# Performance work log

Hardware: AMD Instinct MI355X
Metric: run time of the kernel (lower is better)

The kernel has to match this reference:

```python
import jax, jax.numpy as jnp
import numpy as np

B, S, N = 4, 512, 2048
E = 1024          # expanded_size
QL, H, D, VL = 32, 8, 2, 32   # query_len, num_heads, num_duplicates, values_len
EPS = 1e-5


def setup_inputs() -> dict:
    key = jax.random.key(0)
    ks = jax.random.split(key, 8)
    return {
        "embeddings": jax.random.normal(ks[0], (B, S, E), jnp.float32),
        "keys": jax.random.normal(ks[1], (B, N, QL * H), jnp.float32),
        "values": jax.random.normal(ks[2], (B, N, VL * H), jnp.float32),
        "output_connectivity_sub": jax.random.normal(ks[3], (H, S * D, N), jnp.float32),
        "Wq": jax.random.normal(ks[4], (QL * H * D, E), jnp.float32) / np.sqrt(E),
        "bq": jnp.zeros((QL * H * D,), jnp.float32),
        "Wo": jax.random.normal(ks[5], (E, VL * H * D), jnp.float32) / np.sqrt(VL * H * D),
        "bo": jnp.zeros((E,), jnp.float32),
        "gamma": jnp.ones((VL * H * D,), jnp.float32),
        "beta": jnp.zeros((VL * H * D,), jnp.float32),
    }


def reference(embeddings, keys, values, output_connectivity_sub,
              Wq, bq, Wo, bo, gamma, beta):
    # query projection: [B,S,E] -> [B,S,QL*H*D]
    q = embeddings @ Wq.T + bq
    # view [B, S*D, QL*H] -> [B, S*D, QL, H] -> [B, H, S*D, QL]
    q = q.reshape(B, S * D, QL, H).transpose(0, 3, 1, 2)
    # keys: [B,N,QL*H] -> [B,N,QL,H] -> [B,H,QL,N]
    k = keys.reshape(B, N, QL, H).transpose(0, 3, 2, 1)
    # values: [B,N,VL*H] -> [B,N,VL,H] -> [B,H,N,VL]
    v = values.reshape(B, N, VL, H).transpose(0, 3, 1, 2)

    scores = jnp.einsum('bhsq,bhqn->bhsn', q, k) / np.sqrt(QL).astype(np.float32)
    probs = jax.nn.softmax(scores - output_connectivity_sub, axis=-1)
    vo = jnp.einsum('bhsn,bhnv->bhsv', probs, v)          # [B,H,S*D,VL]

    # [B,H,S*D,VL] -> [B,H,S,VL*D] -> [B,S,H,VL*D] -> [B,S,H*VL*D]
    vo = vo.reshape(B, H, S, VL * D).transpose(0, 2, 1, 3).reshape(B, S, H * VL * D)

    mean = jnp.mean(vo, axis=-1, keepdims=True)
    var = jnp.mean(jnp.square(vo - mean), axis=-1, keepdims=True)
    xn = (vo - mean) / jnp.sqrt(var + EPS) * gamma + beta
    return xn @ Wo.T + bo
```

## Files before the change

### kernel.cpp

```cpp
#include <hip/hip_runtime.h>
#include <hip/hip_bf16.h>


typedef short  short8 __attribute__((ext_vector_type(8)));
typedef float  f32x4  __attribute__((ext_vector_type(4)));

__device__ __forceinline__ ushort f2bf(float x) {
  union { float f; unsigned int u; } v; v.f = x;
  unsigned int r = v.u + 0x7fffu + ((v.u >> 16) & 1u);
  return (ushort)(r >> 16);
}

__device__ __forceinline__ unsigned int cvtpk(float a, float b) {
  unsigned int r;
  asm("v_cvt_pk_bf16_f32 %0, %1, %2" : "=v"(r) : "v"(a), "v"(b));
  return r;
}
__device__ __forceinline__ short8 cvt8(f32x4 a, f32x4 b) {
  union { unsigned int u[4]; short8 s; } r;
  r.u[0] = cvtpk(a[0], a[1]);
  r.u[1] = cvtpk(a[2], a[3]);
  r.u[2] = cvtpk(b[0], b[1]);
  r.u[3] = cvtpk(b[2], b[3]);
  return r.s;
}

#if __has_builtin(__builtin_amdgcn_global_load_lds)
#define OCS_ASYNC 1
__device__ __forceinline__ void gl_lds16(const float* g, float* l) {
  __builtin_amdgcn_global_load_lds(
      (const __attribute__((address_space(1))) unsigned int*)g,
      (__attribute__((address_space(3))) unsigned int*)l, 16, 0, 0);
}
#else
#define OCS_ASYNC 0
#endif

__global__ __launch_bounds__(256) void prep_kv(
    const float* __restrict__ keys, const float* __restrict__ values,
    ushort* __restrict__ kbf, ushort* __restrict__ vbf)
{
  __shared__ ushort T[32][264];
  const int bi = blockIdx.x;
  const int b  = bi >> 6;
  const int n0 = (bi & 63) * 32;
  const int t  = threadIdx.x;
  const int nr = t >> 3;
  const int c0 = (t & 7) * 32;

  {
    const float* src = keys + ((size_t)b*2048 + n0 + nr)*256 + c0;
#pragma unroll
    for (int j = 0; j < 32; j += 8) {
      f32x4 x0 = *(const f32x4*)(src + j);
      f32x4 x1 = *(const f32x4*)(src + j + 4);
      *(short8*)&T[nr][c0 + j] = cvt8(x0, x1);
    }
  }
  __syncthreads();
  {
    const int h = t >> 5, nn = t & 31;
    const int pp = 16*((nn >> 2) & 1) + 4*(nn >> 3) + (nn & 3);
    ushort* dst = kbf + (((size_t)(b*8 + h) * 2048) + n0 + pp) * 32;
#pragma unroll
    for (int j = 0; j < 4; j++) {
      short8 w;
#pragma unroll
      for (int i = 0; i < 8; i++) w[i] = (short)T[nn][(j*8 + i)*8 + h];
      *(short8*)(dst + j*8) = w;
    }
  }
  __syncthreads();
  {
    const float* src = values + ((size_t)b*2048 + n0 + nr)*256 + c0;
#pragma unroll
    for (int j = 0; j < 32; j += 8) {
      f32x4 x0 = *(const f32x4*)(src + j);
      f32x4 x1 = *(const f32x4*)(src + j + 4);
      *(short8*)&T[nr][c0 + j] = cvt8(x0, x1);
    }
  }
  __syncthreads();
  {
    const int c = t, h = c & 7, vl = c >> 3;
    ushort* dst = vbf + (((size_t)(b*8 + h) * 32) + vl) * 2048 + n0;
#pragma unroll
    for (int j = 0; j < 4; j++) {
      short8 w;
#pragma unroll
      for (int i = 0; i < 8; i++) w[i] = (short)T[j*8 + i][c];
      *(short8*)(dst + j*8) = w;
    }
  }
}

template<int EPI>
__global__ __launch_bounds__(256) void gemm_nt(
    const float* __restrict__ A, const float* __restrict__ Bm,
    const float* __restrict__ bias, void* __restrict__ outp,
    int M, int N, int K)
{
  __shared__ ushort As[64][32];
  __shared__ ushort Bs[64][32];
  const int tid = threadIdx.x;
  const int m0 = blockIdx.x * 64;
  const int n0 = blockIdx.y * 64;
  const int lane = tid & 63;
  const int wid  = tid >> 6;
  const int wm = wid >> 1, wn = wid & 1;
  const int lt = lane & 15, g = lane >> 4;
  const int lrow = tid >> 2;
  const int lseg = tid & 3;
  const int slot_w = lseg ^ ((lrow & 3) ^ ((lrow >> 2) & 3));

  f32x4 acc[2][2] = {};

  for (int k0 = 0; k0 < K; k0 += 32) {
    {
      const float* sa = A + (size_t)(m0 + lrow) * K + k0 + lseg * 8;
      f32x4 a0 = *(const f32x4*)sa;
      f32x4 a1 = *(const f32x4*)(sa + 4);
      *(short8*)&As[lrow][slot_w * 8] = cvt8(a0, a1);
      const float* sb = Bm + (size_t)(n0 + lrow) * K + k0 + lseg * 8;
      f32x4 b0 = *(const f32x4*)sb;
      f32x4 b1 = *(const f32x4*)(sb + 4);
      *(short8*)&Bs[lrow][slot_w * 8] = cvt8(b0, b1);
    }
    __syncthreads();
    short8 af[2], bfr[2];
#pragma unroll
    for (int ss = 0; ss < 2; ss++) {
      const int ra = wm*32 + ss*16 + lt;
      af[ss]  = *(const short8*)&As[ra][(g ^ ((ra & 3) ^ ((ra >> 2) & 3))) * 8];
      const int rb = wn*32 + ss*16 + lt;
      bfr[ss] = *(const short8*)&Bs[rb][(g ^ ((rb & 3) ^ ((rb >> 2) & 3))) * 8];
    }
#pragma unroll
    for (int i = 0; i < 2; i++)
#pragma unroll
      for (int j = 0; j < 2; j++)
        acc[i][j] = __builtin_amdgcn_mfma_f32_16x16x32_bf16(af[i], bfr[j], acc[i][j], 0, 0, 0);
    __syncthreads();
  }

#pragma unroll
  for (int i = 0; i < 2; i++)
#pragma unroll
    for (int j = 0; j < 2; j++) {
      const int n  = n0 + wn*32 + j*16 + lt;
      const float bv = bias[n];
      const int mb = m0 + wm*32 + i*16 + g*4;
#pragma unroll
      for (int r = 0; r < 4; r++) {
        const int mm = mb + r;
        if (EPI == 0) {
          const float val = (acc[i][j][r] + bv) * 0.17677669529663687f;
          const int bb = mm >> 9, s = mm & 511;
          const int d = n >> 8, ql = (n >> 3) & 31, hh = n & 7;
          const int tt = s*2 + d;
          ((ushort*)outp)[((size_t)(bb*8 + hh) * 1024 + tt) * 32 + ql] = f2bf(val);
        } else {
          ((float*)outp)[(size_t)mm * N + n] = acc[i][j][r] + bv;
        }
      }
    }
}

__global__ __launch_bounds__(256) void attn_kernel(
    const ushort* __restrict__ qbf, const ushort* __restrict__ kbf,
    const ushort* __restrict__ vbf, const float* __restrict__ ocs,
    float* __restrict__ pacc, float* __restrict__ pl, int nsteps)
{
  __shared__ float obuf0[1024];
  __shared__ float obuf1[1024];
  const int tid  = threadIdx.x;
  const int lane = tid & 63;
  const int c  = blockIdx.x >> 8;
  const int bi = blockIdx.x & 255;
  const int wid = bi * 4 + (tid >> 6);
  const int b  = wid & 3;
  const int tt = (wid >> 2) & 31;
  const int h  = wid >> 7;
  const int t0 = tt * 32;
  const int lt = lane & 15, g = lane >> 4;
  const int n_start = c * nsteps * 32;

  const ushort* qp = qbf + (size_t)(b*8 + h) * (1024*32);
  const ushort* kp = kbf + (size_t)(b*8 + h) * (2048*32);
  const ushort* vp = vbf + (size_t)(b*8 + h) * (32*2048);
  const float*  op = ocs + (size_t)h * (1024*2048);

  const int srow = tid >> 3;
  const int scol = 4 * ((tid & 7) ^ (srow & 7));
  const float* sb = op + (size_t)(t0 + srow) * 2048 + scol;
#if OCS_ASYNC
  const int ldsw = (tid & 192) * 16;
#define SL_ISSUE(BUF, NN) gl_lds16(sb + (NN), (float*)((char*)(BUF) + ldsw))
#define SL_WRITE(BUF)
#define STEP_SYNC(BUFN) do {                                                  \
    __builtin_amdgcn_sched_barrier(0);                                        \
    asm volatile("s_waitcnt vmcnt(4)" ::: "memory");                          \
    __builtin_amdgcn_sched_barrier(0);                                        \
    __builtin_amdgcn_s_barrier();                                             \
  } while (0)
#else
  f32x4 rstage;
#define SL_ISSUE(BUF, NN) rstage = *(const f32x4*)(sb + (NN))
#define SL_WRITE(BUF) *(f32x4*)((char*)(BUF) + (size_t)tid * 16) = rstage
#define STEP_SYNC(BUFN) do { SL_WRITE(BUFN); __syncthreads(); } while (0)
#endif
  const int ro0 = lt * 128;
  const int ro1 = (16 + lt) * 128;
  const int c0x = ((2*g)     ^ (lane & 7)) * 16;
  const int c1x = ((2*g + 1) ^ (lane & 7)) * 16;

  short8 qf[2];
#pragma unroll
  for (int ts = 0; ts < 2; ts++)
    qf[ts] = *(const short8*)(qp + (t0 + ts*16 + lt)*32 + g*8);

  f32x4 acc[2][2] = {};
  float lsum[2] = {0.f, 0.f};
  const f32x4 fzero = {0.f, 0.f, 0.f, 0.f};

  short8 ck0 = *(const short8*)(kp + (n_start + lt)*32 + g*8);
  short8 ck1 = *(const short8*)(kp + (n_start + 16 + lt)*32 + g*8);
  short8 cv0 = *(const short8*)(vp + (lt)*2048 + n_start + g*8);
  short8 cv1 = *(const short8*)(vp + (16 + lt)*2048 + n_start + g*8);

  SL_ISSUE(obuf0, n_start);
  SL_WRITE(obuf0);
  __syncthreads();

#define STEP(BUFC, BUFN, NNEXT, NSTAGE) do {                                  \
    SL_ISSUE(BUFN, (NSTAGE));                                                 \
    __builtin_amdgcn_sched_barrier(0);                                        \
    f32x4 co[2][2];                                                           \
    co[0][0] = *(const f32x4*)((const char*)(BUFC) + ro0 + c0x);              \
    co[1][0] = *(const f32x4*)((const char*)(BUFC) + ro0 + c1x);              \
    co[0][1] = *(const f32x4*)((const char*)(BUFC) + ro1 + c0x);              \
    co[1][1] = *(const f32x4*)((const char*)(BUFC) + ro1 + c1x);              \
    short8 nk0 = *(const short8*)(kp + ((NNEXT) + lt)*32 + g*8);              \
    short8 nk1 = *(const short8*)(kp + ((NNEXT) + 16 + lt)*32 + g*8);         \
    short8 nv0 = *(const short8*)(vp + (lt)*2048 + (NNEXT) + g*8);            \
    short8 nv1 = *(const short8*)(vp + (16 + lt)*2048 + (NNEXT) + g*8);       \
    f32x4 sc0[2], sc1[2];                                                     \
    _Pragma("unroll")                                                         \
    for (int ts = 0; ts < 2; ts++) {                                          \
      sc0[ts] = __builtin_amdgcn_mfma_f32_16x16x32_bf16(ck0, qf[ts], fzero, 0, 0, 0); \
      sc1[ts] = __builtin_amdgcn_mfma_f32_16x16x32_bf16(ck1, qf[ts], fzero, 0, 0, 0); \
    }                                                                         \
    _Pragma("unroll")                                                         \
    for (int ts = 0; ts < 2; ts++) {                                          \
      float p0 = __expf(sc0[ts][0] - co[0][ts][0]);             \
      float p1 = __expf(sc0[ts][1] - co[0][ts][1]);             \
      float p2 = __expf(sc0[ts][2] - co[0][ts][2]);             \
      float p3 = __expf(sc0[ts][3] - co[0][ts][3]);             \
      float p4 = __expf(sc1[ts][0] - co[1][ts][0]);             \
      float p5 = __expf(sc1[ts][1] - co[1][ts][1]);             \
      float p6 = __expf(sc1[ts][2] - co[1][ts][2]);             \
      float p7 = __expf(sc1[ts][3] - co[1][ts][3]);             \
      lsum[ts] += ((p0+p1)+(p2+p3)) + ((p4+p5)+(p6+p7));                      \
      union { unsigned int u[4]; short8 s; } pf;                              \
      pf.u[0] = (unsigned int)f2bf(p0) | ((unsigned int)f2bf(p1) << 16);      \
      pf.u[1] = (unsigned int)f2bf(p2) | ((unsigned int)f2bf(p3) << 16);      \
      pf.u[2] = (unsigned int)f2bf(p4) | ((unsigned int)f2bf(p5) << 16);      \
      pf.u[3] = (unsigned int)f2bf(p6) | ((unsigned int)f2bf(p7) << 16);      \
      acc[ts][0] = __builtin_amdgcn_mfma_f32_16x16x32_bf16(cv0, pf.s, acc[ts][0], 0, 0, 0); \
      acc[ts][1] = __builtin_amdgcn_mfma_f32_16x16x32_bf16(cv1, pf.s, acc[ts][1], 0, 0, 0); \
    }                                                                         \
    STEP_SYNC(BUFN);                                                          \
    ck0 = nk0; ck1 = nk1; cv0 = nv0; cv1 = nv1;                               \
  } while (0)

  for (int i = 0; i < nsteps; i += 2) {
    const int n1 = (i + 1 < nsteps) ? n_start + (i+1)*32 : n_start;
    const int n2 = (i + 2 < nsteps) ? n_start + (i+2)*32 : n_start;
    STEP(obuf0, obuf1, n1, n1);
    STEP(obuf1, obuf0, n2, n2);
  }
#undef STEP
#undef STEP_SYNC
#undef SL_ISSUE
#undef SL_WRITE

  {
    float* pb = pacc + ((size_t)(c*1024 + wid) * 4) * 256 + lane * 4;
#pragma unroll
    for (int ts = 0; ts < 2; ts++)
#pragma unroll
      for (int vs = 0; vs < 2; vs++)
        *(f32x4*)(pb + (ts*2 + vs) * 256) = acc[ts][vs];
  }
#pragma unroll
  for (int ts = 0; ts < 2; ts++) {
    float L = lsum[ts];
    L += __shfl_xor(L, 16);
    L += __shfl_xor(L, 32);
    if (g == 0) pl[((size_t)(c*1024 + wid)) * 32 + ts*16 + lt] = L;
  }
}

__global__ __launch_bounds__(256) void combine_kernel(
    const float* __restrict__ pacc, const float* __restrict__ pl,
    float* __restrict__ vo, int NS)
{
  const int lane = threadIdx.x & 63;
  const int wid = blockIdx.x * 4 + (threadIdx.x >> 6);
  const int b  = wid & 3;
  const int tt = (wid >> 2) & 31;
  const int h  = wid >> 7;
  const int t0 = tt * 32;
  const int lt = lane & 15, g = lane >> 4;

  f32x4 acc[4] = {};
  float L[2] = {0.f, 0.f};
  for (int cc = 0; cc < NS; ++cc) {
    const float* pb = pacc + ((size_t)(cc*1024 + wid) * 4) * 256 + lane * 4;
#pragma unroll
    for (int q = 0; q < 4; q++) {
      f32x4 v = *(const f32x4*)(pb + q * 256);
#pragma unroll
      for (int r = 0; r < 4; r++) acc[q][r] += v[r];
    }
    L[0] += pl[((size_t)(cc*1024 + wid)) * 32 + lt];
    L[1] += pl[((size_t)(cc*1024 + wid)) * 32 + 16 + lt];
  }
#pragma unroll
  for (int ts = 0; ts < 2; ts++) {
    const float inv = 1.0f / L[ts];
    const int t = t0 + ts*16 + lt;
    const int s = t >> 1, d = t & 1;
    float* dst = vo + ((size_t)(b*512 + s) * 512) + h*64 + d*32;
#pragma unroll
    for (int vs = 0; vs < 2; vs++) {
      f32x4 o;
#pragma unroll
      for (int r = 0; r < 4; r++) o[r] = acc[ts*2 + vs][r] * inv;
      *(f32x4*)(dst + vs*16 + g*4) = o;
    }
  }
}

__global__ __launch_bounds__(256) void ln_kernel(
    const float* __restrict__ x_in, const float* __restrict__ gamma,
    const float* __restrict__ beta, float* __restrict__ x_out)
{
  const int row  = blockIdx.x * 4 + (threadIdx.x >> 6);
  const int lane = threadIdx.x & 63;
  const float* x = x_in + (size_t)row * 512 + lane * 8;
  f32x4 v0 = *(const f32x4*)x;
  f32x4 v1 = *(const f32x4*)(x + 4);
  float s = (v0[0]+v0[1]+v0[2]+v0[3]) + (v1[0]+v1[1]+v1[2]+v1[3]);
#pragma unroll
  for (int off = 1; off < 64; off <<= 1) s += __shfl_xor(s, off);
  const float mean = s * (1.0f/512.0f);
  float var = 0.f;
#pragma unroll
  for (int i = 0; i < 4; i++) {
    float d0 = v0[i]-mean, d1 = v1[i]-mean;
    var += d0*d0 + d1*d1;
  }
#pragma unroll
  for (int off = 1; off < 64; off <<= 1) var += __shfl_xor(var, off);
  const float rstd = rsqrtf(var * (1.0f/512.0f) + 1e-5f);
  const float* gp = gamma + lane*8;
  const float* bp = beta  + lane*8;
  f32x4 g0 = *(const f32x4*)gp, g1 = *(const f32x4*)(gp+4);
  f32x4 b0 = *(const f32x4*)bp, b1 = *(const f32x4*)(bp+4);
  f32x4 o0, o1;
#pragma unroll
  for (int i = 0; i < 4; i++) {
    o0[i] = (v0[i]-mean)*rstd*g0[i] + b0[i];
    o1[i] = (v1[i]-mean)*rstd*g1[i] + b1[i];
  }
  float* o = x_out + (size_t)row * 512 + lane * 8;
  *(f32x4*)o = o0;
  *(f32x4*)(o + 4) = o1;
}

extern "C" void kernel_launch(void* const* d_in, const int* in_sizes, int n_in,
                              void* d_out, int out_size, void* d_ws, size_t ws_size,
                              hipStream_t stream)
{
  const float* emb    = (const float*)d_in[0];
  const float* keys   = (const float*)d_in[1];
  const float* values = (const float*)d_in[2];
  const float* ocs    = (const float*)d_in[3];
  const float* Wq     = (const float*)d_in[4];
  const float* bq     = (const float*)d_in[5];
  const float* Wo     = (const float*)d_in[6];
  const float* bo     = (const float*)d_in[7];
  const float* gamma  = (const float*)d_in[8];
  const float* beta   = (const float*)d_in[9];

  char* ws = (char*)d_ws;
  ushort* qbf = (ushort*)(ws);
  ushort* kbf = (ushort*)(ws + (2u << 20));
  ushort* vbf = (ushort*)(ws + (6u << 20));
  float*  vo  = (float*) (ws + (10u << 20));
  const size_t pbase = (size_t)14u << 20;

  int NS;
  if      (ws_size >= ((size_t)48u << 20)) NS = 8;
  else if (ws_size >= ((size_t)31u << 20)) NS = 4;
  else if (ws_size >= ((size_t)23u << 20)) NS = 2;
  else                                     NS = 1;
  float* pacc = (float*)(ws + pbase);
  float* pl   = (float*)(ws + pbase + (size_t)NS * (4u << 20));
  const int nsteps = 2048 / (NS * 32);

  prep_kv<<<dim3(256), dim3(256), 0, stream>>>(keys, values, kbf, vbf);
  gemm_nt<0><<<dim3(32, 8), dim3(256), 0, stream>>>(emb, Wq, bq, (void*)qbf, 2048, 512, 1024);
  attn_kernel<<<dim3(256 * NS), dim3(256), 0, stream>>>(qbf, kbf, vbf, ocs, pacc, pl, nsteps);
  combine_kernel<<<dim3(256), dim3(256), 0, stream>>>(pacc, pl, vo, NS);
  ln_kernel<<<dim3(512), dim3(256), 0, stream>>>(vo, gamma, beta, vo);
  gemm_nt<1><<<dim3(32, 16), dim3(256), 0, stream>>>(vo, Wo, bo, d_out, 2048, 1024, 512);
}
```

Before: 97.92 us.

## Deepen attention pipeline: process step pairs with 8-slot LDS ring buffer

```diff
diff --git a/kernel.cpp b/kernel.cpp
--- a/kernel.cpp
+++ b/kernel.cpp
@@ -171,8 +171,9 @@
     const ushort* __restrict__ vbf, const float* __restrict__ ocs,
     float* __restrict__ pacc, float* __restrict__ pl, int nsteps)
 {
-  __shared__ float obuf0[1024];
-  __shared__ float obuf1[1024];
+#if OCS_ASYNC
+  __shared__ float obuf[8][1024];
+#endif
   const int tid  = threadIdx.x;
   const int lane = tid & 63;
   const int c  = blockIdx.x >> 8;
@@ -190,29 +191,52 @@
   const ushort* vp = vbf + (size_t)(b*8 + h) * (32*2048);
   const float*  op = ocs + (size_t)h * (1024*2048);
 
+#define NSX(I) (((I) < nsteps) ? (n_start + (I)*32) : n_start)
+
   const int srow = tid >> 3;
   const int scol = 4 * ((tid & 7) ^ (srow & 7));
   const float* sb = op + (size_t)(t0 + srow) * 2048 + scol;
 #if OCS_ASYNC
   const int ldsw = (tid & 192) * 16;
-#define SL_ISSUE(BUF, NN) gl_lds16(sb + (NN), (float*)((char*)(BUF) + ldsw))
-#define SL_WRITE(BUF)
-#define STEP_SYNC(BUFN) do {                                                  \
+#define SL_ISSUE(STEP) gl_lds16(sb + NSX(STEP), \
+    (float*)((char*)obuf + (((STEP) & 7) << 12) + ldsw))
+  const int ro0 = lt * 128;
+  const int ro1 = (16 + lt) * 128;
+  const int c0x = ((2*g)     ^ (lt & 7)) * 16;
+  const int c1x = ((2*g + 1) ^ (lt & 7)) * 16;
+#define CO_READ(DST, STEP) do {                                               \
+    const char* bb_ = (const char*)obuf + (((STEP) & 7) << 12);               \
+    DST[0][0] = *(const f32x4*)(bb_ + ro0 + c0x);                             \
+    DST[1][0] = *(const f32x4*)(bb_ + ro0 + c1x);                             \
+    DST[0][1] = *(const f32x4*)(bb_ + ro1 + c0x);                             \
+    DST[1][1] = *(const f32x4*)(bb_ + ro1 + c1x);                             \
+  } while (0)
+#define PAIR_SYNC() do {                                                      \
     __builtin_amdgcn_sched_barrier(0);                                        \
-    asm volatile("s_waitcnt vmcnt(4)" ::: "memory");                          \
+    asm volatile("s_waitcnt vmcnt(10)" ::: "memory");                         \
     __builtin_amdgcn_sched_barrier(0);                                        \
     __builtin_amdgcn_s_barrier();                                             \
   } while (0)
 #else
-  f32x4 rstage;
-#define SL_ISSUE(BUF, NN) rstage = *(const f32x4*)(sb + (NN))
-#define SL_WRITE(BUF) *(f32x4*)((char*)(BUF) + (size_t)tid * 16) = rstage
-#define STEP_SYNC(BUFN) do { SL_WRITE(BUFN); __syncthreads(); } while (0)
+  const float* opr0 = op + (size_t)(t0 + lt) * 2048;
+  const float* opr1 = op + (size_t)(t0 + 16 + lt) * 2048;
+#define SL_ISSUE(STEP)
+#define CO_READ(DST, STEP) do {                                               \
+    const int nn_ = NSX(STEP);                                                \
+    DST[0][0] = *(const f32x4*)(opr0 + nn_ + 8*g);                            \
+    DST[1][0] = *(const f32x4*)(opr0 + nn_ + 8*g + 4);                        \
+    DST[0][1] = *(const f32x4*)(opr1 + nn_ + 8*g);                            \
+    DST[1][1] = *(const f32x4*)(opr1 + nn_ + 8*g + 4);                        \
+  } while (0)
+#define PAIR_SYNC()
 #endif
-  const int ro0 = lt * 128;
-  const int ro1 = (16 + lt) * 128;
-  const int c0x = ((2*g)     ^ (lane & 7)) * 16;
-  const int c1x = ((2*g + 1) ^ (lane & 7)) * 16;
+
+#define LD_KV(KD, VD, NN) do {                                                \
+    KD[0] = *(const short8*)(kp + (size_t)((NN) + lt) * 32 + g*8);            \
+    KD[1] = *(const short8*)(kp + (size_t)((NN) + 16 + lt) * 32 + g*8);       \
+    VD[0] = *(const short8*)(vp + (size_t)lt * 2048 + (NN) + g*8);            \
+    VD[1] = *(const short8*)(vp + (size_t)(16 + lt) * 2048 + (NN) + g*8);     \
+  } while (0)
 
   short8 qf[2];
 #pragma unroll
@@ -223,66 +247,72 @@
   float lsum[2] = {0.f, 0.f};
   const f32x4 fzero = {0.f, 0.f, 0.f, 0.f};
 
-  short8 ck0 = *(const short8*)(kp + (n_start + lt)*32 + g*8);
-  short8 ck1 = *(const short8*)(kp + (n_start + 16 + lt)*32 + g*8);
-  short8 cv0 = *(const short8*)(vp + (lt)*2048 + n_start + g*8);
-  short8 cv1 = *(const short8*)(vp + (16 + lt)*2048 + n_start + g*8);
-
-  SL_ISSUE(obuf0, n_start);
-  SL_WRITE(obuf0);
-  __syncthreads();
-
-#define STEP(BUFC, BUFN, NNEXT, NSTAGE) do {                                  \
-    SL_ISSUE(BUFN, (NSTAGE));                                                 \
+#define TSB(SC0, SC1, CO0, CO1, VLO, VHI, LS, ACCA, ACCB) do {                \
+    float p0 = __expf(SC0[0] - CO0[0]);                                       \
+    float p1 = __expf(SC0[1] - CO0[1]);                                       \
+    float p2 = __expf(SC0[2] - CO0[2]);                                       \
+    float p3 = __expf(SC0[3] - CO0[3]);                                       \
+    float p4 = __expf(SC1[0] - CO1[0]);                                       \
+    float p5 = __expf(SC1[1] - CO1[1]);                                       \
+    float p6 = __expf(SC1[2] - CO1[2]);                                       \
+    float p7 = __expf(SC1[3] - CO1[3]);                                       \
+    LS += ((p0+p1)+(p2+p3)) + ((p4+p5)+(p6+p7));                              \
+    union { unsigned int u[4]; short8 s; } pf;                                \
+    pf.u[0] = (unsigned int)f2bf(p0) | ((unsigned int)f2bf(p1) << 16);        \
+    pf.u[1] = (unsigned int)f2bf(p2) | ((unsigned int)f2bf(p3) << 16);        \
+    pf.u[2] = (unsigned int)f2bf(p4) | ((unsigned int)f2bf(p5) << 16);        \
+    pf.u[3] = (unsigned int)f2bf(p6) | ((unsigned int)f2bf(p7) << 16);        \
+    ACCA = __builtin_amdgcn_mfma_f32_16x16x32_bf16(VLO, pf.s, ACCA, 0, 0, 0); \
+    ACCB = __builtin_amdgcn_mfma_f32_16x16x32_bf16(VHI, pf.s, ACCB, 0, 0, 0); \
+  } while (0)
+
+#define PAIR(SA_, KC, VC, KN, VN) do {                                        \
+    const int sA_ = (SA_);                                                    \
+    LD_KV(KN[0], VN[0], NSX(sA_ + 2));                                        \
+    LD_KV(KN[1], VN[1], NSX(sA_ + 3));                                        \
+    SL_ISSUE(sA_ + 4);                                                        \
+    SL_ISSUE(sA_ + 5);                                                        \
     __builtin_amdgcn_sched_barrier(0);                                        \
-    f32x4 co[2][2];                                                           \
-    co[0][0] = *(const f32x4*)((const char*)(BUFC) + ro0 + c0x);              \
-    co[1][0] = *(const f32x4*)((const char*)(BUFC) + ro0 + c1x);              \
-    co[0][1] = *(const f32x4*)((const char*)(BUFC) + ro1 + c0x);              \
-    co[1][1] = *(const f32x4*)((const char*)(BUFC) + ro1 + c1x);              \
-    short8 nk0 = *(const short8*)(kp + ((NNEXT) + lt)*32 + g*8);              \
-    short8 nk1 = *(const short8*)(kp + ((NNEXT) + 16 + lt)*32 + g*8);         \
-    short8 nv0 = *(const short8*)(vp + (lt)*2048 + (NNEXT) + g*8);            \
-    short8 nv1 = *(const short8*)(vp + (16 + lt)*2048 + (NNEXT) + g*8);       \
-    f32x4 sc0[2], sc1[2];                                                     \
+    f32x4 coA[2][2], coB[2][2];                                               \
+    CO_READ(coA, sA_);                                                        \
+    CO_READ(coB, sA_ + 1);                                                    \
+    f32x4 scA0[2], scA1[2], scB0[2], scB1[2];                                 \
     _Pragma("unroll")                                                         \
     for (int ts = 0; ts < 2; ts++) {                                          \
-      sc0[ts] = __builtin_amdgcn_mfma_f32_16x16x32_bf16(ck0, qf[ts], fzero, 0, 0, 0); \
-      sc1[ts] = __builtin_amdgcn_mfma_f32_16x16x32_bf16(ck1, qf[ts], fzero, 0, 0, 0); \
+      scA0[ts] = __builtin_amdgcn_mfma_f32_16x16x32_bf16(KC[0][0], qf[ts], fzero, 0, 0, 0); \
+      scA1[ts] = __builtin_amdgcn_mfma_f32_16x16x32_bf16(KC[0][1], qf[ts], fzero, 0, 0, 0); \
+      scB0[ts] = __builtin_amdgcn_mfma_f32_16x16x32_bf16(KC[1][0], qf[ts], fzero, 0, 0, 0); \
+      scB1[ts] = __builtin_amdgcn_mfma_f32_16x16x32_bf16(KC[1][1], qf[ts], fzero, 0, 0, 0); \
     }                                                                         \
-    _Pragma("unroll")                                                         \
-    for (int ts = 0; ts < 2; ts++) {                                          \
-      float p0 = __expf(sc0[ts][0] - co[0][ts][0]);             \
-      float p1 = __expf(sc0[ts][1] - co[0][ts][1]);             \
-      float p2 = __expf(sc0[ts][2] - co[0][ts][2]);             \
-      float p3 = __expf(sc0[ts][3] - co[0][ts][3]);             \
-      float p4 = __expf(sc1[ts][0] - co[1][ts][0]);             \
-      float p5 = __expf(sc1[ts][1] - co[1][ts][1]);             \
-      float p6 = __expf(sc1[ts][2] - co[1][ts][2]);             \
-      float p7 = __expf(sc1[ts][3] - co[1][ts][3]);             \
-      lsum[ts] += ((p0+p1)+(p2+p3)) + ((p4+p5)+(p6+p7));                      \
-      union { unsigned int u[4]; short8 s; } pf;                              \
-      pf.u[0] = (unsigned int)f2bf(p0) | ((unsigned int)f2bf(p1) << 16);      \
-      pf.u[1] = (unsigned int)f2bf(p2) | ((unsigned int)f2bf(p3) << 16);      \
-      pf.u[2] = (unsigned int)f2bf(p4) | ((unsigned int)f2bf(p5) << 16);      \
-      pf.u[3] = (unsigned int)f2bf(p6) | ((unsigned int)f2bf(p7) << 16);      \
-      acc[ts][0] = __builtin_amdgcn_mfma_f32_16x16x32_bf16(cv0, pf.s, acc[ts][0], 0, 0, 0); \
-      acc[ts][1] = __builtin_amdgcn_mfma_f32_16x16x32_bf16(cv1, pf.s, acc[ts][1], 0, 0, 0); \
-    }                                                                         \
-    STEP_SYNC(BUFN);                                                          \
-    ck0 = nk0; ck1 = nk1; cv0 = nv0; cv1 = nv1;                               \
-  } while (0)
-
-  for (int i = 0; i < nsteps; i += 2) {
-    const int n1 = (i + 1 < nsteps) ? n_start + (i+1)*32 : n_start;
-    const int n2 = (i + 2 < nsteps) ? n_start + (i+2)*32 : n_start;
-    STEP(obuf0, obuf1, n1, n1);
-    STEP(obuf1, obuf0, n2, n2);
-  }
-#undef STEP
-#undef STEP_SYNC
+    TSB(scA0[0], scA1[0], coA[0][0], coA[1][0], VC[0][0], VC[0][1], lsum[0], acc[0][0], acc[0][1]); \
+    TSB(scB0[0], scB1[0], coB[0][0], coB[1][0], VC[1][0], VC[1][1], lsum[0], acc[0][0], acc[0][1]); \
+    TSB(scA0[1], scA1[1], coA[0][1], coA[1][1], VC[0][0], VC[0][1], lsum[1], acc[1][0], acc[1][1]); \
+    TSB(scB0[1], scB1[1], coB[0][1], coB[1][1], VC[1][0], VC[1][1], lsum[1], acc[1][0], acc[1][1]); \
+    PAIR_SYNC();                                                              \
+  } while (0)
+
+  short8 KA[2][2], VA[2][2], KB[2][2], VB[2][2];
+
+  LD_KV(KA[0], VA[0], NSX(0));
+  LD_KV(KA[1], VA[1], NSX(1));
+#if OCS_ASYNC
+  SL_ISSUE(0); SL_ISSUE(1); SL_ISSUE(2); SL_ISSUE(3);
+  __builtin_amdgcn_sched_barrier(0);
+  asm volatile("s_waitcnt vmcnt(2)" ::: "memory");
+  __builtin_amdgcn_s_barrier();
+#endif
+
+  for (int s = 0; s < nsteps; s += 4) {
+    PAIR(s,     KA, VA, KB, VB);
+    PAIR(s + 2, KB, VB, KA, VA);
+  }
+#undef PAIR
+#undef TSB
+#undef LD_KV
+#undef CO_READ
 #undef SL_ISSUE
-#undef SL_WRITE
+#undef PAIR_SYNC
+#undef NSX
 
   {
     float* pb = pacc + ((size_t)(c*1024 + wid) * 4) * 256 + lane * 4;
@@ -402,8 +432,7 @@
   const size_t pbase = (size_t)14u << 20;
 
   int NS;
-  if      (ws_size >= ((size_t)48u << 20)) NS = 8;
-  else if (ws_size >= ((size_t)31u << 20)) NS = 4;
+  if      (ws_size >= ((size_t)31u << 20)) NS = 4;
   else if (ws_size >= ((size_t)23u << 20)) NS = 2;
   else                                     NS = 1;
   float* pacc = (float*)(ws + pbase);
```

New measurement: 101.4 us. 3.5% more time.
